# Kernel tuning notes

Measured on AMD Instinct MI355X. Metric: run time of the kernel, lower is better.

The kernel has to match this reference:

```python
import jax, jax.numpy as jnp
import numpy as np

TOPK = 2
ROUTED_SCALING_FACTOR = 1.0


def setup_inputs() -> dict:
    key = jax.random.key(0)
    k1, k2 = jax.random.split(key)
    N, D, E = 8192, 4096, 64
    x = jax.random.normal(k1, (N, D), dtype=jnp.float32)
    expert_embeddings = jax.random.normal(k2, (E, D), dtype=jnp.float32) * 0.02
    gate_bias = jnp.zeros((E,), dtype=jnp.float32)
    return {"x": x, "expert_embeddings": expert_embeddings, "gate_bias": gate_bias}


def reference(x, expert_embeddings, gate_bias):
    # logits: (N, E) = x @ W^T, computed in fp32 as in the original
    logits = jnp.einsum('nd,ed->ne', x.astype(jnp.float32), expert_embeddings.astype(jnp.float32))
    scores = jax.nn.sigmoid(logits)
    biased_scores = scores + gate_bias  # bias only affects expert selection
    _, indices = jax.lax.top_k(biased_scores, TOPK)  # (N, topk)
    weights = jnp.take_along_axis(scores, indices, axis=-1)  # gather unbiased scores
    weights = weights / jnp.sum(weights, axis=-1, keepdims=True)
    weights = weights * ROUTED_SCALING_FACTOR
    return weights, indices, scores
```

## Files before the change

### kernel.cpp

```cpp
#include <hip/hip_runtime.h>
#include <hip/hip_bf16.h>
#include <math.h>

#define NROWS 8192
#define DDIM  4096
#define NEXP  64
#define KSPLIT 16
#define KCHUNK (DDIM / KSPLIT)
#define KSTEPS (KCHUNK / 32)

typedef __attribute__((ext_vector_type(8))) short bf16x8;
typedef __attribute__((ext_vector_type(4))) float f32x4;

__device__ inline unsigned short bf16_rne(float f) {
    unsigned u = __builtin_bit_cast(unsigned, f);
    u += 0x7FFF + ((u >> 16) & 1);
    return (unsigned short)(u >> 16);
}

__device__ inline void split8(const float* xf, bf16x8& hi, bf16x8& lo) {
#pragma unroll
    for (int j = 0; j < 8; j++) {
        const unsigned short h = bf16_rne(xf[j]);
        const float hf = __builtin_bit_cast(float, (unsigned)h << 16);
        hi[j] = (short)h;
        lo[j] = (short)bf16_rne(xf[j] - hf);
    }
}

__global__ __launch_bounds__(256) void wfrag_kernel(
    const float* __restrict__ w, unsigned short* __restrict__ whi,
    unsigned short* __restrict__ wlo, float* __restrict__ logits)
{
    const int kc = blockIdx.x;
    const int t  = threadIdx.x >> 6;
    const int l  = threadIdx.x & 63;
    const int e  = t * 16 + (l & 15);
    const int k0 = kc * 32 + ((l >> 4) * 8);
    const float* p = w + (size_t)e * DDIM + k0;
    float xf[8];
    *(float4*)&xf[0] = *(const float4*)p;
    *(float4*)&xf[4] = *(const float4*)(p + 4);
    bf16x8 hi, lo;
    split8(xf, hi, lo);
    const size_t off = ((size_t)(kc * 4 + t) * 64 + l) * 8;
    *(bf16x8*)(whi + off) = hi;
    *(bf16x8*)(wlo + off) = lo;

    const float4 z = {0.f, 0.f, 0.f, 0.f};
    float4* lz = (float4*)logits;
    const int base = (blockIdx.x * 256 + threadIdx.x) * 4;
#pragma unroll
    for (int j = 0; j < 4; j++) lz[base + j] = z;
}

__global__ __launch_bounds__(256) void gemm_partial_kernel(
    const float* __restrict__ x, const unsigned short* __restrict__ whi,
    const unsigned short* __restrict__ wlo, float* __restrict__ logits)
{
    const int tid = threadIdx.x;
    const int wv  = tid >> 6;
    const int l   = tid & 63;
    const int q   = l >> 4;
    const int col = l & 15;
    const int r0  = blockIdx.x * 128 + wv * 32;
    const int kh  = blockIdx.y;
    const int kb  = kh * KCHUNK;

    const float* xp0 = x + (size_t)(r0 + col) * DDIM + kb + q * 8;
    const float* xp1 = xp0 + (size_t)16 * DDIM;
    const unsigned short* bhp = whi + ((size_t)(kb / 32) * 4 * 64 + l) * 8;
    const unsigned short* blp = wlo + ((size_t)(kb / 32) * 4 * 64 + l) * 8;

    f32x4 acc[2][4];
#pragma unroll
    for (int m = 0; m < 2; m++)
#pragma unroll
        for (int t = 0; t < 4; t++) acc[m][t] = f32x4{0, 0, 0, 0};

    float xf[2][2][8];
    *(float4*)&xf[0][0][0] = *(const float4*)(xp0);
    *(float4*)&xf[0][0][4] = *(const float4*)(xp0 + 4);
    *(float4*)&xf[0][1][0] = *(const float4*)(xp1);
    *(float4*)&xf[0][1][4] = *(const float4*)(xp1 + 4);

    for (int s = 0; s < KSTEPS; s++) {
        const int cur = s & 1, nxt = cur ^ 1;

        if (s + 1 < KSTEPS) {
            const float* xn0 = xp0 + (s + 1) * 32;
            const float* xn1 = xp1 + (s + 1) * 32;
            *(float4*)&xf[nxt][0][0] = *(const float4*)(xn0);
            *(float4*)&xf[nxt][0][4] = *(const float4*)(xn0 + 4);
            *(float4*)&xf[nxt][1][0] = *(const float4*)(xn1);
            *(float4*)&xf[nxt][1][4] = *(const float4*)(xn1 + 4);
        }

        bf16x8 bh[4], bl[4];
        const unsigned short* bhs = bhp + (size_t)s * 4 * 64 * 8;
        const unsigned short* bls = blp + (size_t)s * 4 * 64 * 8;
#pragma unroll
        for (int t = 0; t < 4; t++) {
            bh[t] = *(const bf16x8*)(bhs + (size_t)t * 64 * 8);
            bl[t] = *(const bf16x8*)(bls + (size_t)t * 64 * 8);
        }

        bf16x8 ah[2], al[2];
        split8(xf[cur][0], ah[0], al[0]);
        split8(xf[cur][1], ah[1], al[1]);
#pragma unroll
        for (int m = 0; m < 2; m++)
#pragma unroll
            for (int t = 0; t < 4; t++) {
                acc[m][t] = __builtin_amdgcn_mfma_f32_16x16x32_bf16(ah[m], bh[t], acc[m][t], 0, 0, 0);
                acc[m][t] = __builtin_amdgcn_mfma_f32_16x16x32_bf16(ah[m], bl[t], acc[m][t], 0, 0, 0);
                acc[m][t] = __builtin_amdgcn_mfma_f32_16x16x32_bf16(al[m], bh[t], acc[m][t], 0, 0, 0);
            }
    }

#pragma unroll
    for (int m = 0; m < 2; m++)
#pragma unroll
        for (int t = 0; t < 4; t++)
#pragma unroll
            for (int r = 0; r < 4; r++)
                unsafeAtomicAdd(
                    &logits[(size_t)(r0 + m * 16 + q * 4 + r) * NEXP + t * 16 + col],
                    acc[m][t][r]);
}

__global__ __launch_bounds__(256) void gate_topk_kernel(
    const float* __restrict__ logits, const float* __restrict__ bias,
    float* __restrict__ out)
{
    const int tid = threadIdx.x;
    const int e   = tid & 63;
    const int row = blockIdx.x * 4 + (tid >> 6);
    const size_t idx = (size_t)row * NEXP + e;

    const float be    = bias[e];
    const float logit = logits[idx];
    const float score = 1.0f / (1.0f + expf(-logit));
    out[(size_t)4 * NROWS + idx] = score;

    const float biased = score + be;

    float v = biased; int bi = e;
#pragma unroll
    for (int off = 32; off; off >>= 1) {
        const float ov = __shfl_xor(v, off);
        const int   oi = __shfl_xor(bi, off);
        if (ov > v || (ov == v && oi < bi)) { v = ov; bi = oi; }
    }
    const int i1 = bi;

    float v2 = (e == i1) ? -INFINITY : biased;
    int bi2 = e;
#pragma unroll
    for (int off = 32; off; off >>= 1) {
        const float ov = __shfl_xor(v2, off);
        const int   oi = __shfl_xor(bi2, off);
        if (ov > v2 || (ov == v2 && oi < bi2)) { v2 = ov; bi2 = oi; }
    }
    const int i2 = bi2;

    const float s1 = __shfl(score, i1);
    const float s2 = __shfl(score, i2);
    if (e == 0) {
        const float inv = 1.0f / (s1 + s2);
        out[(size_t)row * 2 + 0] = s1 * inv;
        out[(size_t)row * 2 + 1] = s2 * inv;
        out[(size_t)2 * NROWS + row * 2 + 0] = (float)i1;
        out[(size_t)2 * NROWS + row * 2 + 1] = (float)i2;
    }
}

extern "C" void kernel_launch(void* const* d_in, const int* in_sizes, int n_in,
                              void* d_out, int out_size, void* d_ws, size_t ws_size,
                              hipStream_t stream)
{
    const float* x    = (const float*)d_in[0];
    const float* w    = (const float*)d_in[1];
    const float* bias = (const float*)d_in[2];
    float* out  = (float*)d_out;

    float* logits = (float*)d_ws;
    const size_t logits_bytes = (size_t)NROWS * NEXP * 4;
    unsigned short* whi = (unsigned short*)((char*)d_ws + logits_bytes);
    unsigned short* wlo = whi + (size_t)NEXP * DDIM;

    wfrag_kernel<<<DDIM / 32, 256, 0, stream>>>(w, whi, wlo, logits);
    dim3 g1(NROWS / 128, KSPLIT);
    gemm_partial_kernel<<<g1, 256, 0, stream>>>(x, whi, wlo, logits);
    gate_topk_kernel<<<NROWS / 4, 256, 0, stream>>>(logits, bias, out);
}
```

Baseline: 217.8 us.

## Stage x tiles via global_load_lds into swizzled double-buffered LDS

```diff
diff --git a/kernel.cpp b/kernel.cpp
--- a/kernel.cpp
+++ b/kernel.cpp
@@ -58,17 +58,22 @@
     const float* __restrict__ x, const unsigned short* __restrict__ whi,
     const unsigned short* __restrict__ wlo, float* __restrict__ logits)
 {
+    __shared__ float ldsx[4 * 2 * 1024];
+
     const int tid = threadIdx.x;
     const int wv  = tid >> 6;
     const int l   = tid & 63;
     const int q   = l >> 4;
     const int col = l & 15;
+    const int c7  = col & 7;
     const int r0  = blockIdx.x * 128 + wv * 32;
-    const int kh  = blockIdx.y;
-    const int kb  = kh * KCHUNK;
-
-    const float* xp0 = x + (size_t)(r0 + col) * DDIM + kb + q * 8;
-    const float* xp1 = xp0 + (size_t)16 * DDIM;
+    const int kb  = blockIdx.y * KCHUNK;
+
+    const int slr   = l >> 3;
+    const int slotp = l & 7;
+
+    float* ldsw = ldsx + wv * 2048;
+
     const unsigned short* bhp = whi + ((size_t)(kb / 32) * 4 * 64 + l) * 8;
     const unsigned short* blp = wlo + ((size_t)(kb / 32) * 4 * 64 + l) * 8;
 
@@ -78,23 +83,24 @@
 #pragma unroll
         for (int t = 0; t < 4; t++) acc[m][t] = f32x4{0, 0, 0, 0};
 
-    float xf[2][2][8];
-    *(float4*)&xf[0][0][0] = *(const float4*)(xp0);
-    *(float4*)&xf[0][0][4] = *(const float4*)(xp0 + 4);
-    *(float4*)&xf[0][1][0] = *(const float4*)(xp1);
-    *(float4*)&xf[0][1][4] = *(const float4*)(xp1 + 4);
+    auto STAGE = [&](int buf, int s) {
+#pragma unroll
+        for (int g = 0; g < 4; g++) {
+            const int lr   = g * 8 + slr;
+            const int slot = slotp ^ (lr & 7);
+            const float* gp = x + (size_t)(r0 + lr) * DDIM + kb + s * 32 + slot * 4;
+            __builtin_amdgcn_global_load_lds(
+                (const __attribute__((address_space(1))) void*)gp,
+                (__attribute__((address_space(3))) void*)(ldsw + buf * 1024 + g * 256),
+                16, 0, 0);
+        }
+    };
+
+    STAGE(0, 0);
+    __builtin_amdgcn_sched_barrier(0);
 
     for (int s = 0; s < KSTEPS; s++) {
-        const int cur = s & 1, nxt = cur ^ 1;
-
-        if (s + 1 < KSTEPS) {
-            const float* xn0 = xp0 + (s + 1) * 32;
-            const float* xn1 = xp1 + (s + 1) * 32;
-            *(float4*)&xf[nxt][0][0] = *(const float4*)(xn0);
-            *(float4*)&xf[nxt][0][4] = *(const float4*)(xn0 + 4);
-            *(float4*)&xf[nxt][1][0] = *(const float4*)(xn1);
-            *(float4*)&xf[nxt][1][4] = *(const float4*)(xn1 + 4);
-        }
+        const int buf = s & 1;
 
         bf16x8 bh[4], bl[4];
         const unsigned short* bhs = bhp + (size_t)s * 4 * 64 * 8;
@@ -105,9 +111,24 @@
             bl[t] = *(const bf16x8*)(bls + (size_t)t * 64 * 8);
         }
 
+        asm volatile("s_waitcnt vmcnt(8)" ::: "memory");
+        __builtin_amdgcn_sched_barrier(0);
+
+        float xr[2][8];
+#pragma unroll
+        for (int m = 0; m < 2; m++) {
+            const float* rb = ldsw + buf * 1024 + (m * 16 + col) * 32;
+            const int sp0 = (q * 2) ^ c7;
+            *(float4*)&xr[m][0] = *(const float4*)(rb + sp0 * 4);
+            *(float4*)&xr[m][4] = *(const float4*)(rb + (sp0 ^ 1) * 4);
+        }
+
+        STAGE(buf ^ 1, (s + 1) & 7);
+        __builtin_amdgcn_sched_barrier(0);
+
         bf16x8 ah[2], al[2];
-        split8(xf[cur][0], ah[0], al[0]);
-        split8(xf[cur][1], ah[1], al[1]);
+        split8(xr[0], ah[0], al[0]);
+        split8(xr[1], ah[1], al[1]);
 #pragma unroll
         for (int m = 0; m < 2; m++)
 #pragma unroll
```

Measured after the change: 213.7 us. About the same (-1.9%).
